# Optimization experiments

Hardware: AMD Instinct MI355X
Metric: run time of the kernel (lower is better)

## Reference

```python
import jax, jax.numpy as jnp
import numpy as np

M_MARGIN = 0.5
SCALE = 64.0
COS_M = float(np.cos(M_MARGIN))
SIN_M = float(np.sin(M_MARGIN))
TH = -COS_M
MM = SIN_M * M_MARGIN
NUM_CLASSES = 100000
IN_FEATURES = 512
BATCH = 512


def setup_inputs() -> dict:
    key = jax.random.key(0)
    k1, k2, k3 = jax.random.split(key, 3)
    x = jax.random.normal(k1, (BATCH, IN_FEATURES), dtype=jnp.float32)
    y = jax.random.randint(k2, (BATCH,), 0, NUM_CLASSES, dtype=jnp.int64 if jax.config.jax_enable_x64 else jnp.int32)
    # xavier_uniform-like init for weight [num_classes, in_features]
    limit = float(np.sqrt(6.0 / (NUM_CLASSES + IN_FEATURES)))
    weight = jax.random.uniform(k3, (NUM_CLASSES, IN_FEATURES), minval=-limit, maxval=limit, dtype=jnp.float32)
    return {"x": x, "y": y, "weight": weight}


def _l2_normalize(v, axis=-1, eps=1e-12):
    # matches F.normalize(p=2): v / max(||v||, eps)
    n = jnp.sqrt(jnp.sum(v * v, axis=axis, keepdims=True))
    return v / jnp.maximum(n, eps)


def reference(x, y, weight):
    # cosine logits: [B, C]
    xn = _l2_normalize(x)
    wn = _l2_normalize(weight)
    cos = jnp.einsum('bd,cd->bc', xn, wn)
    sin = jnp.sqrt(jnp.clip(1.0 - cos * cos, 0.0))
    cos_w_margin = cos * COS_M - sin * SIN_M
    cos_w_margin = jnp.where(cos > TH, cos_w_margin, cos - MM)
    ohe = jax.nn.one_hot(y, NUM_CLASSES, dtype=jnp.bool_)
    logit = jnp.where(ohe, cos_w_margin, cos) * SCALE
    # cross entropy, mean reduction
    logp = jax.nn.log_softmax(logit, axis=-1)
    nll = -jnp.take_along_axis(logp, y[:, None], axis=-1)[:, 0]
    return jnp.mean(nll)
```

## Files before the change

kernel.cpp:

```cpp
#include <hip/hip_runtime.h>
#include <hip/hip_bf16.h>
#include <cstdint>
#include <cstddef>

#define C_CLS   100000
#define D_FEAT  512
#define B_ROWS  512
#define NBN     782

#define COSM 0.8775825618903728f
#define SINM 0.479425538604203f
#define TH_  (-0.8775825618903728f)
#define MM_  0.2397127693021015f

typedef __bf16 bf16x8 __attribute__((ext_vector_type(8)));
typedef __bf16 bf16x4 __attribute__((ext_vector_type(4)));
typedef float  f32x4  __attribute__((ext_vector_type(4)));

typedef __attribute__((address_space(3))) void lds_void;
typedef const __attribute__((address_space(1))) void g_void;

__device__ __forceinline__ void async_copy16(const void* g, void* l) {
    __builtin_amdgcn_global_load_lds((g_void*)g, (lds_void*)l, 16, 0, 0);
}

__global__ void k_xnorm(const float* __restrict__ x, __bf16* __restrict__ xn,
                        float* __restrict__ out) {
    const int row  = blockIdx.x;
    const int lane = threadIdx.x;
    if (row == 0 && lane == 0) out[0] = 0.0f;
    const f32x4* p = (const f32x4*)(x + (size_t)row * D_FEAT);
    f32x4 a = p[lane];
    f32x4 b = p[lane + 64];
    float s = a[0]*a[0] + a[1]*a[1] + a[2]*a[2] + a[3]*a[3]
            + b[0]*b[0] + b[1]*b[1] + b[2]*b[2] + b[3]*b[3];
    #pragma unroll
    for (int m = 32; m >= 1; m >>= 1) s += __shfl_xor(s, m, 64);
    const float inv = 1.0f / fmaxf(sqrtf(s), 1e-12f);
    bf16x4 o0 = { (__bf16)(a[0]*inv), (__bf16)(a[1]*inv), (__bf16)(a[2]*inv), (__bf16)(a[3]*inv) };
    bf16x4 o1 = { (__bf16)(b[0]*inv), (__bf16)(b[1]*inv), (__bf16)(b[2]*inv), (__bf16)(b[3]*inv) };
    *(bf16x4*)(xn + (size_t)row * D_FEAT + lane * 4)       = o0;
    *(bf16x4*)(xn + (size_t)row * D_FEAT + 256 + lane * 4) = o1;
}

__global__ void k_wnorm(const float* __restrict__ w, __bf16* __restrict__ wn) {
    const int row  = blockIdx.x * 4 + (threadIdx.x >> 6);
    const int lane = threadIdx.x & 63;
    const f32x4* p = (const f32x4*)(w + (size_t)row * D_FEAT);
    f32x4 a = p[lane * 2];
    f32x4 b = p[lane * 2 + 1];
    float s = a[0]*a[0] + a[1]*a[1] + a[2]*a[2] + a[3]*a[3]
            + b[0]*b[0] + b[1]*b[1] + b[2]*b[2] + b[3]*b[3];
    #pragma unroll
    for (int m = 32; m >= 1; m >>= 1) s += __shfl_xor(s, m, 64);
    const float inv = 1.0f / fmaxf(sqrtf(s), 1e-12f);
    bf16x8 o;
    o[0] = (__bf16)(a[0]*inv); o[1] = (__bf16)(a[1]*inv);
    o[2] = (__bf16)(a[2]*inv); o[3] = (__bf16)(a[3]*inv);
    o[4] = (__bf16)(b[0]*inv); o[5] = (__bf16)(b[1]*inv);
    o[6] = (__bf16)(b[2]*inv); o[7] = (__bf16)(b[3]*inv);
    *(bf16x8*)(wn + (size_t)row * D_FEAT + lane * 8) = o;
}

__global__ __launch_bounds__(256, 4) void k_gemm(
        const __bf16* __restrict__ xn, const __bf16* __restrict__ wn,
        const int* __restrict__ y,
        float* __restrict__ psum, float* __restrict__ tlogit) {

    __shared__ __align__(16) __bf16 As[2][4096];
    __shared__ __align__(16) __bf16 Bs[2][4096];
    __shared__ int   ys[128];
    __shared__ float red[2][128];

    const int tid = threadIdx.x;
    const int wg = (blockIdx.x & 7) * (4 * NBN / 8) + (blockIdx.x >> 3);
    const int bm = wg & 3;
    const int bn = wg >> 2;

    if (tid < 128) ys[tid] = y[bm * 128 + tid];

    const int wave = tid >> 6;
    const int lane = tid & 63;
    const int wm   = wave >> 1;
    const int wn_  = wave & 1;
    const int quad = lane >> 4;
    const int l15  = lane & 15;

    f32x4 acc[4][4];
    #pragma unroll
    for (int i = 0; i < 4; ++i)
        #pragma unroll
        for (int j = 0; j < 4; ++j) acc[i][j] = (f32x4){0.f, 0.f, 0.f, 0.f};

    #define STAGE(s, kt_) do {                                                          \
        const int k0_ = (kt_) * 32;                                                     \
        _Pragma("unroll")                                                               \
        for (int i_ = 0; i_ < 2; ++i_) {                                                \
            const int c_ = tid + i_ * 256;                                              \
            const int qc_ = c_ >> 7, rc_ = c_ & 127;                                    \
            async_copy16(xn + (size_t)(bm * 128 + rc_) * D_FEAT + k0_ + qc_ * 8,        \
                         &As[s][c_ * 8]);                                               \
        }                                                                               \
        _Pragma("unroll")                                                               \
        for (int i_ = 0; i_ < 2; ++i_) {                                                \
            const int c_ = tid + i_ * 256;                                              \
            const int qc_ = c_ >> 7, rc_ = c_ & 127;                                    \
            int grow_ = bn * 128 + rc_; if (grow_ > C_CLS - 1) grow_ = C_CLS - 1;       \
            async_copy16(wn + (size_t)grow_ * D_FEAT + k0_ + qc_ * 8,                   \
                         &Bs[s][c_ * 8]);                                               \
        }                                                                               \
    } while (0)

    STAGE(0, 0);
    STAGE(1, 1);

    #pragma unroll
    for (int kt = 0; kt < 16; ++kt) {
        const int cur = kt & 1;

        if (kt < 15) asm volatile("s_waitcnt vmcnt(4)" ::: "memory");
        else         asm volatile("s_waitcnt vmcnt(0)" ::: "memory");
        __builtin_amdgcn_s_barrier();

        bf16x8 af[4];
        #pragma unroll
        for (int mi = 0; mi < 4; ++mi)
            af[mi] = *(const bf16x8*)&As[cur][(quad * 128 + wm * 64 + mi * 16 + l15) * 8];
        bf16x8 bfr[4];
        #pragma unroll
        for (int ni = 0; ni < 4; ++ni)
            bfr[ni] = *(const bf16x8*)&Bs[cur][(quad * 128 + wn_ * 64 + ni * 16 + l15) * 8];

        asm volatile("s_waitcnt lgkmcnt(0)" ::: "memory");
        __builtin_amdgcn_s_barrier();
        if (kt < 14) STAGE(cur, kt + 2);

        #pragma unroll
        for (int mi = 0; mi < 4; ++mi)
            #pragma unroll
            for (int ni = 0; ni < 4; ++ni)
                acc[mi][ni] = __builtin_amdgcn_mfma_f32_16x16x32_bf16(af[mi], bfr[ni], acc[mi][ni], 0, 0, 0);
    }
    #undef STAGE

    #pragma unroll
    for (int mi = 0; mi < 4; ++mi) {
        float rs[4] = {0.f, 0.f, 0.f, 0.f};
        #pragma unroll
        for (int ni = 0; ni < 4; ++ni) {
            const int gcol = bn * 128 + wn_ * 64 + ni * 16 + l15;
            const bool colv = (gcol < C_CLS);
            #pragma unroll
            for (int reg = 0; reg < 4; ++reg) {
                const int lrow = wm * 64 + mi * 16 + quad * 4 + reg;
                const float cosv = acc[mi][ni][reg];
                const float sinv = sqrtf(fmaxf(1.0f - cosv * cosv, 0.0f));
                const float phi  = (cosv > TH_) ? (cosv * COSM - sinv * SINM) : (cosv - MM_);
                const bool ist   = colv && (gcol == ys[lrow]);
                const float logit = 64.0f * (ist ? phi : cosv);
                if (ist) tlogit[bm * 128 + lrow] = logit;
                rs[reg] += colv ? __expf(logit - 64.0f) : 0.0f;
            }
        }
        #pragma unroll
        for (int reg = 0; reg < 4; ++reg) {
            float v = rs[reg];
            v += __shfl_xor(v, 8, 64);
            v += __shfl_xor(v, 4, 64);
            v += __shfl_xor(v, 2, 64);
            v += __shfl_xor(v, 1, 64);
            if (l15 == 0) red[wn_][wm * 64 + mi * 16 + quad * 4 + reg] = v;
        }
    }
    __syncthreads();
    if (tid < 128) {
        const float v = red[0][tid] + red[1][tid];
        psum[(size_t)(bm * 128 + tid) * NBN + bn] = v;
    }
}

__global__ void k_final(const float* __restrict__ psum, const float* __restrict__ tlogit,
                        float* __restrict__ out) {
    const int row = blockIdx.x * 4 + (threadIdx.x >> 6);
    const int l   = threadIdx.x & 63;
    const float* p = psum + (size_t)row * NBN;
    float s = 0.0f;
    for (int i = l; i < NBN; i += 64) s += p[i];
    #pragma unroll
    for (int m = 32; m >= 1; m >>= 1) s += __shfl_xor(s, m, 64);
    if (l == 0) {
        const float loss = logf(s) + 64.0f - tlogit[row];
        atomicAdd(out, loss * (1.0f / 512.0f));
    }
}

extern "C" void kernel_launch(void* const* d_in, const int* in_sizes, int n_in,
                              void* d_out, int out_size, void* d_ws, size_t ws_size,
                              hipStream_t stream) {
    const float* x = (const float*)d_in[0];
    const int*   y = (const int*)d_in[1];
    const float* w = (const float*)d_in[2];

    char* ws = (char*)d_ws;
    __bf16* xn     = (__bf16*)ws;
    float*  psum   = (float*)(ws + 524288);
    float*  tlogit = (float*)(ws + 524288 + 1601536);
    __bf16* wn     = (__bf16*)(ws + 524288 + 1601536 + 2048);
    float*  out    = (float*)d_out;

    hipLaunchKernelGGL(k_xnorm, dim3(512), dim3(64), 0, stream, x, xn, out);
    hipLaunchKernelGGL(k_wnorm, dim3(25000), dim3(256), 0, stream, w, wn);
    hipLaunchKernelGGL(k_gemm, dim3(4 * NBN), dim3(256), 0, stream, xn, wn, y, psum, tlogit);
    hipLaunchKernelGGL(k_final, dim3(128), dim3(256), 0, stream, psum, tlogit, out);
}
```

Baseline: 435.1 us.

## Merge norm kernels and fold final reduction into GEMM via last-block atomics

Combines the x and weight normalization kernels into one launch and removes the separate final-reduction kernel. GEMM blocks now atomically add per-row partial sums into a 512-entry buffer, and a global counter picks the last block to compute the log-sum-exp loss. This drops two kernel launches and the psum round trip through memory. In exchange it adds contended float atomics on 512 addresses and an extra sync per block, and the final loss is computed by a single block.

```diff
diff --git a/kernel.cpp b/kernel.cpp
--- a/kernel.cpp
+++ b/kernel.cpp
@@ -7,6 +7,7 @@
 #define D_FEAT  512
 #define B_ROWS  512
 #define NBN     782
+#define NBLK    (4 * NBN)
 
 #define COSM 0.8775825618903728f
 #define SINM 0.479425538604203f
@@ -14,7 +15,6 @@
 #define MM_  0.2397127693021015f
 
 typedef __bf16 bf16x8 __attribute__((ext_vector_type(8)));
-typedef __bf16 bf16x4 __attribute__((ext_vector_type(4)));
 typedef float  f32x4  __attribute__((ext_vector_type(4)));
 
 typedef __attribute__((address_space(3))) void lds_void;
@@ -24,29 +24,21 @@
     __builtin_amdgcn_global_load_lds((g_void*)g, (lds_void*)l, 16, 0, 0);
 }
 
-__global__ void k_xnorm(const float* __restrict__ x, __bf16* __restrict__ xn,
-                        float* __restrict__ out) {
-    const int row  = blockIdx.x;
-    const int lane = threadIdx.x;
-    if (row == 0 && lane == 0) out[0] = 0.0f;
-    const f32x4* p = (const f32x4*)(x + (size_t)row * D_FEAT);
-    f32x4 a = p[lane];
-    f32x4 b = p[lane + 64];
-    float s = a[0]*a[0] + a[1]*a[1] + a[2]*a[2] + a[3]*a[3]
-            + b[0]*b[0] + b[1]*b[1] + b[2]*b[2] + b[3]*b[3];
-    #pragma unroll
-    for (int m = 32; m >= 1; m >>= 1) s += __shfl_xor(s, m, 64);
-    const float inv = 1.0f / fmaxf(sqrtf(s), 1e-12f);
-    bf16x4 o0 = { (__bf16)(a[0]*inv), (__bf16)(a[1]*inv), (__bf16)(a[2]*inv), (__bf16)(a[3]*inv) };
-    bf16x4 o1 = { (__bf16)(b[0]*inv), (__bf16)(b[1]*inv), (__bf16)(b[2]*inv), (__bf16)(b[3]*inv) };
-    *(bf16x4*)(xn + (size_t)row * D_FEAT + lane * 4)       = o0;
-    *(bf16x4*)(xn + (size_t)row * D_FEAT + 256 + lane * 4) = o1;
-}
-
-__global__ void k_wnorm(const float* __restrict__ w, __bf16* __restrict__ wn) {
-    const int row  = blockIdx.x * 4 + (threadIdx.x >> 6);
+__global__ void k_norm(const float* __restrict__ x, const float* __restrict__ w,
+                       __bf16* __restrict__ xn, __bf16* __restrict__ wn,
+                       float* __restrict__ row_sum, int* __restrict__ counter) {
+    const int r4   = blockIdx.x * 4 + (threadIdx.x >> 6);
     const int lane = threadIdx.x & 63;
-    const f32x4* p = (const f32x4*)(w + (size_t)row * D_FEAT);
+    const float* src;
+    __bf16*      dst;
+    if (r4 < C_CLS) {
+        src = w  + (size_t)r4 * D_FEAT;
+        dst = wn + (size_t)r4 * D_FEAT;
+    } else {
+        src = x  + (size_t)(r4 - C_CLS) * D_FEAT;
+        dst = xn + (size_t)(r4 - C_CLS) * D_FEAT;
+    }
+    const f32x4* p = (const f32x4*)src;
     f32x4 a = p[lane * 2];
     f32x4 b = p[lane * 2 + 1];
     float s = a[0]*a[0] + a[1]*a[1] + a[2]*a[2] + a[3]*a[3]
@@ -59,21 +51,30 @@
     o[2] = (__bf16)(a[2]*inv); o[3] = (__bf16)(a[3]*inv);
     o[4] = (__bf16)(b[0]*inv); o[5] = (__bf16)(b[1]*inv);
     o[6] = (__bf16)(b[2]*inv); o[7] = (__bf16)(b[3]*inv);
-    *(bf16x8*)(wn + (size_t)row * D_FEAT + lane * 8) = o;
+    *(bf16x8*)(dst + lane * 8) = o;
+
+    if (blockIdx.x == C_CLS / 4) {
+        row_sum[threadIdx.x]       = 0.0f;
+        row_sum[threadIdx.x + 256] = 0.0f;
+        if (threadIdx.x == 0) *counter = 0;
+    }
 }
 
 __global__ __launch_bounds__(256, 4) void k_gemm(
         const __bf16* __restrict__ xn, const __bf16* __restrict__ wn,
         const int* __restrict__ y,
-        float* __restrict__ psum, float* __restrict__ tlogit) {
+        float* __restrict__ row_sum, float* __restrict__ tlogit,
+        int* __restrict__ counter, float* __restrict__ out) {
 
     __shared__ __align__(16) __bf16 As[2][4096];
     __shared__ __align__(16) __bf16 Bs[2][4096];
     __shared__ int   ys[128];
     __shared__ float red[2][128];
+    __shared__ int   lastflag;
+    __shared__ float pr[4];
 
     const int tid = threadIdx.x;
-    const int wg = (blockIdx.x & 7) * (4 * NBN / 8) + (blockIdx.x >> 3);
+    const int wg = (blockIdx.x & 7) * (NBLK / 8) + (blockIdx.x >> 3);
     const int bm = wg & 3;
     const int bn = wg >> 2;
 
@@ -158,7 +159,7 @@
                 const float phi  = (cosv > TH_) ? (cosv * COSM - sinv * SINM) : (cosv - MM_);
                 const bool ist   = colv && (gcol == ys[lrow]);
                 const float logit = 64.0f * (ist ? phi : cosv);
-                if (ist) tlogit[bm * 128 + lrow] = logit;
+                if (ist) atomicExch(&tlogit[bm * 128 + lrow], logit);
                 rs[reg] += colv ? __expf(logit - 64.0f) : 0.0f;
             }
         }
@@ -175,22 +176,30 @@
     __syncthreads();
     if (tid < 128) {
         const float v = red[0][tid] + red[1][tid];
-        psum[(size_t)(bm * 128 + tid) * NBN + bn] = v;
-    }
-}
-
-__global__ void k_final(const float* __restrict__ psum, const float* __restrict__ tlogit,
-                        float* __restrict__ out) {
-    const int row = blockIdx.x * 4 + (threadIdx.x >> 6);
-    const int l   = threadIdx.x & 63;
-    const float* p = psum + (size_t)row * NBN;
-    float s = 0.0f;
-    for (int i = l; i < NBN; i += 64) s += p[i];
-    #pragma unroll
-    for (int m = 32; m >= 1; m >>= 1) s += __shfl_xor(s, m, 64);
-    if (l == 0) {
-        const float loss = logf(s) + 64.0f - tlogit[row];
-        atomicAdd(out, loss * (1.0f / 512.0f));
+        atomicAdd(&row_sum[bm * 128 + tid], v);
+    }
+
+    __syncthreads();
+    if (tid == 0) {
+        const int t = atomicAdd(counter, 1);
+        lastflag = (t == NBLK - 1) ? 1 : 0;
+    }
+    __syncthreads();
+    if (lastflag) {
+        float part = 0.0f;
+        #pragma unroll
+        for (int i = 0; i < 2; ++i) {
+            const int row = tid + i * 256;
+            const float rsv = atomicAdd(&row_sum[row], 0.0f);
+            const float tlv = atomicAdd(&tlogit[row], 0.0f);
+            part += logf(rsv) + 64.0f - tlv;
+        }
+        #pragma unroll
+        for (int m = 32; m >= 1; m >>= 1) part += __shfl_xor(part, m, 64);
+        if ((tid & 63) == 0) pr[tid >> 6] = part;
+        __syncthreads();
+        if (tid == 0)
+            out[0] = (pr[0] + pr[1] + pr[2] + pr[3]) * (1.0f / 512.0f);
     }
 }
 
@@ -202,14 +211,15 @@
     const float* w = (const float*)d_in[2];
 
     char* ws = (char*)d_ws;
-    __bf16* xn     = (__bf16*)ws;
-    float*  psum   = (float*)(ws + 524288);
-    float*  tlogit = (float*)(ws + 524288 + 1601536);
-    __bf16* wn     = (__bf16*)(ws + 524288 + 1601536 + 2048);
-    float*  out    = (float*)d_out;
-
-    hipLaunchKernelGGL(k_xnorm, dim3(512), dim3(64), 0, stream, x, xn, out);
-    hipLaunchKernelGGL(k_wnorm, dim3(25000), dim3(256), 0, stream, w, wn);
-    hipLaunchKernelGGL(k_gemm, dim3(4 * NBN), dim3(256), 0, stream, xn, wn, y, psum, tlogit);
-    hipLaunchKernelGGL(k_final, dim3(128), dim3(256), 0, stream, psum, tlogit, out);
-}
+    __bf16* xn      = (__bf16*)ws;
+    __bf16* wn      = (__bf16*)(ws + 524288);
+    float*  row_sum = (float*)(ws + 524288 + 102400000);
+    float*  tlogit  = (float*)(ws + 524288 + 102400000 + 2048);
+    int*    counter = (int*)(ws + 524288 + 102400000 + 4096);
+    float*  out     = (float*)d_out;
+
+    hipLaunchKernelGGL(k_norm, dim3((C_CLS + B_ROWS) / 4), dim3(256), 0, stream,
+                       x, w, xn, wn, row_sum, counter);
+    hipLaunchKernelGGL(k_gemm, dim3(NBLK), dim3(256), 0, stream,
+                       xn, wn, y, row_sum, tlogit, counter, out);
+}
```

New measurement: 415.6 us (median of 2 runs). -4.5%, faster.
